# Optimization experiments

Hardware: AMD Instinct MI355X
Metric: run time of the kernel (lower is better)

The kernel has to match this reference:

```python
import jax, jax.numpy as jnp
import numpy as np

N_NODES = 10000
N_RAND_EDGES = 320000
IN_DIM = 256
HIDDEN = 64
HEADS = 8
OUT_DIM = 256
NEG_SLOPE = 0.2


def setup_inputs() -> dict:
    key = jax.random.key(0)
    ks = jax.random.split(key, 9)
    h = jax.random.normal(ks[0], (N_NODES, IN_DIM), dtype=jnp.float32)
    # random edges + self-loops so every dst has >=1 incoming edge
    src = jnp.concatenate([
        jax.random.randint(ks[1], (N_RAND_EDGES,), 0, N_NODES, dtype=jnp.int32),
        jnp.arange(N_NODES, dtype=jnp.int32)])
    dst = jnp.concatenate([
        jax.random.randint(ks[2], (N_RAND_EDGES,), 0, N_NODES, dtype=jnp.int32),
        jnp.arange(N_NODES, dtype=jnp.int32)])
    def glorot(k, shape):
        fan = shape[0] + shape[-1]
        s = jnp.sqrt(2.0 / fan).astype(jnp.float32)
        return jax.random.normal(k, shape, dtype=jnp.float32) * s
    W1 = glorot(ks[3], (IN_DIM, HEADS * HIDDEN))
    attn_l1 = glorot(ks[4], (HEADS, HIDDEN))
    attn_r1 = glorot(ks[5], (HEADS, HIDDEN))
    W2 = glorot(ks[6], (HEADS * HIDDEN, OUT_DIM))
    attn_l2 = glorot(ks[7], (1, OUT_DIM))
    attn_r2 = glorot(ks[8], (1, OUT_DIM))
    return {"h": h, "W1": W1, "attn_l1": attn_l1, "attn_r1": attn_r1,
            "W2": W2, "attn_l2": attn_l2, "attn_r2": attn_r2,
            "src": src, "dst": dst}


def gat_conv(x, W, attn_l, attn_r, src, dst, n_nodes):
    # x: [N, F_in]; W: [F_in, H*D]; attn_l/attn_r: [H, D]
    H, D = attn_l.shape
    feat = (x @ W).reshape(n_nodes, H, D)          # [N, H, D]
    el = jnp.einsum('nhd,hd->nh', feat, attn_l)    # [N, H]
    er = jnp.einsum('nhd,hd->nh', feat, attn_r)
    e = jax.nn.leaky_relu(el[src] + er[dst], NEG_SLOPE)  # [E, H]
    # edge softmax over incoming edges of each destination node
    m = jax.ops.segment_max(e, dst, num_segments=n_nodes)      # [N, H]
    ex = jnp.exp(e - m[dst])                                   # [E, H]
    denom = jax.ops.segment_sum(ex, dst, num_segments=n_nodes) # [N, H]
    alpha = ex / denom[dst]                                    # [E, H]
    out = jax.ops.segment_sum(alpha[:, :, None] * feat[src], dst,
                              num_segments=n_nodes)            # [N, H, D]
    return out.reshape(n_nodes, H * D)


def reference(h, W1, attn_l1, attn_r1, W2, attn_l2, attn_r2, src, dst):
    n = h.shape[0]
    x = gat_conv(h, W1, attn_l1, attn_r1, src, dst, n)   # [N, H*hidden]
    x = jax.nn.elu(x)
    out = gat_conv(x, W2, attn_l2, attn_r2, src, dst, n) # [N, out_dim]
    return out
```

## Files before the change

### kernel.cpp

```cpp
#include <hip/hip_runtime.h>
#include <hip/hip_bf16.h>

#define N_NODES 10000
#define IN_DIM 256
#define HID 512
#define HEADS 8
#define OUT_DIM 256
#define NEG 0.2f
#define CAP 128
#define WPREP_BLOCKS (((IN_DIM*HID)+(HID*OUT_DIM))/256)

typedef __hip_bfloat16 bf16;
typedef __attribute__((ext_vector_type(8))) short short8;
typedef __attribute__((ext_vector_type(4))) float f32x4;

__device__ __forceinline__ float ldm(const void* p, long i, int mode){
  if(mode) return ((const float*)p)[i];
  return __bfloat162float(((const bf16*)p)[i]);
}
__device__ __forceinline__ unsigned short f2bf(float f){
  bf16 b = __float2bfloat16(f);
  return *(unsigned short*)&b;
}
__device__ __forceinline__ float bflo(unsigned int u){ return __uint_as_float(u<<16); }
__device__ __forceinline__ float bfhi(unsigned int u){ return __uint_as_float(u&0xffff0000u); }

__global__ void detect_zero_k(const unsigned short* w1raw, int* mode, int* cnt,
                              float* el2, float* er2){
  int t = threadIdx.x;
  if(blockIdx.x==0){
    __shared__ int sbad;
    if(t==0) sbad=0;
    __syncthreads();
    int bad=0;
    for(int i=t;i<512;i+=256){
      unsigned int u = ((unsigned int)w1raw[i])<<16;
      float f = __uint_as_float(u);
      if(!(f==f) || fabsf(f) > 100.0f) bad++;
    }
    #pragma unroll
    for(int o=32;o>0;o>>=1) bad += __shfl_down(bad,o);
    if((t&63)==0) atomicAdd(&sbad, bad);
    __syncthreads();
    if(t==0) *mode = (sbad>10) ? 1 : 0;
  } else {
    int i = (blockIdx.x-1)*256 + t;
    if(i<N_NODES){ cnt[i]=0; el2[i]=0.f; er2[i]=0.f; }
  }
}

__global__ void prep2_k(const void* W1, const void* W2, unsigned short* wt1,
                        unsigned short* wt2, const int* modep,
                        const int* src, const int* dst, int* cnt, int* bucket, int E){
  int b = blockIdx.x, t = threadIdx.x;
  if(b < WPREP_BLOCKS){
    int md = *modep;
    long i = (long)b*256 + t;
    const long n1 = (long)IN_DIM*HID;
    if(i < n1){
      int k = (int)(i/HID), n = (int)(i%HID);
      unsigned short v = md ? f2bf(((const float*)W1)[i]) : ((const unsigned short*)W1)[i];
      wt1[(long)n*IN_DIM + k] = v;
    } else {
      long j = i - n1;
      int k = (int)(j/OUT_DIM), n = (int)(j%OUT_DIM);
      unsigned short v = md ? f2bf(((const float*)W2)[j]) : ((const unsigned short*)W2)[j];
      wt2[(long)n*HID + k] = v;
    }
  } else {
    int e = (b-WPREP_BLOCKS)*256 + t;
    if(e<E){
      int d = dst[e];
      int pos = atomicAdd(&cnt[d], 1);
      if(pos < CAP) bucket[(long)d*CAP + pos] = src[e];
    }
  }
}

__global__ __launch_bounds__(256) void gemm_k(const void* A, const unsigned short* Bt,
                                              unsigned short* C, int M, int N, int K,
                                              int asel, const int* modep,
                                              const void* al, const void* ar,
                                              float* el, float* er, int dmode){
  int md = *modep;
  int am = asel ? md : 0;
  __shared__ short As[64*40];
  __shared__ short Bs[64*40];
  __shared__ float led[64], ler[64];
  int t = threadIdx.x;
  int lane = t & 63, wave = t >> 6;
  int l15 = lane & 15, quad = lane >> 4;
  int wm = (wave>>1)*32, wn = (wave&1)*32;
  int mbase = blockIdx.y*64, nbase = blockIdx.x*64;

  f32x4 acc[2][2];
  #pragma unroll
  for(int i=0;i<2;i++)
    #pragma unroll
    for(int j=0;j<2;j++) acc[i][j] = (f32x4){0.f,0.f,0.f,0.f};

  int row = t>>2, kk = (t&3)*8;
  long arow = (long)(mbase+row)*K, brow = (long)(nbase+row)*K;
  bool av = (mbase+row) < M;
  const unsigned short* Ab = (const unsigned short*)A;
  const float* Af = (const float*)A;

  for(int k0=0;k0<K;k0+=32){
    short8 a = (short8){0,0,0,0,0,0,0,0};
    if(am){
      if(av){
        float4 x = *(const float4*)(Af + arow + k0 + kk);
        float4 y = *(const float4*)(Af + arow + k0 + kk + 4);
        a[0]=f2bf(x.x); a[1]=f2bf(x.y); a[2]=f2bf(x.z); a[3]=f2bf(x.w);
        a[4]=f2bf(y.x); a[5]=f2bf(y.y); a[6]=f2bf(y.z); a[7]=f2bf(y.w);
      }
    } else {
      if(av) a = *(const short8*)(Ab + arow + k0 + kk);
    }
    short8 b = *(const short8*)(Bt + brow + k0 + kk);
    __syncthreads();
    *(short8*)(As + row*40 + kk) = a;
    *(short8*)(Bs + row*40 + kk) = b;
    __syncthreads();
    short8 af[2], bfr[2];
    #pragma unroll
    for(int mi=0;mi<2;mi++) af[mi]  = *(short8*)(As + (wm + mi*16 + l15)*40 + quad*8);
    #pragma unroll
    for(int ni=0;ni<2;ni++) bfr[ni] = *(short8*)(Bs + (wn + ni*16 + l15)*40 + quad*8);
    #pragma unroll
    for(int mi=0;mi<2;mi++)
      #pragma unroll
      for(int ni=0;ni<2;ni++)
        acc[mi][ni] = __builtin_amdgcn_mfma_f32_16x16x32_bf16(af[mi], bfr[ni], acc[mi][ni], 0,0,0);
  }

  #pragma unroll
  for(int mi=0;mi<2;mi++){
    #pragma unroll
    for(int ni=0;ni<2;ni++){
      int grow0 = mbase + wm + mi*16 + quad*4;
      int gcol  = nbase + wn + ni*16 + l15;
      #pragma unroll
      for(int r=0;r<4;r++){
        int grow = grow0 + r;
        if(grow < M) C[(long)grow*N + gcol] = f2bf(acc[mi][ni][r]);
      }
    }
  }

  float avv[2], rvv[2];
  #pragma unroll
  for(int ni=0;ni<2;ni++){
    int gc = nbase + wn + ni*16 + l15;
    avv[ni] = ldm(al, gc, md);
    rvv[ni] = ldm(ar, gc, md);
  }
  __syncthreads();
  if(t<64){ led[t]=0.f; ler[t]=0.f; }
  __syncthreads();
  #pragma unroll
  for(int mi=0;mi<2;mi++){
    #pragma unroll
    for(int r=0;r<4;r++){
      float pl = acc[mi][0][r]*avv[0] + acc[mi][1][r]*avv[1];
      float pr = acc[mi][0][r]*rvv[0] + acc[mi][1][r]*rvv[1];
      #pragma unroll
      for(int o=1;o<16;o<<=1){ pl += __shfl_xor(pl,o); pr += __shfl_xor(pr,o); }
      if(l15==0){
        int lr = wm + mi*16 + quad*4 + r;
        atomicAdd(&led[lr], pl);
        atomicAdd(&ler[lr], pr);
      }
    }
  }
  __syncthreads();
  if(t<64){
    int grow = mbase + t;
    if(grow < M){
      if(dmode==1){
        el[(long)grow*HEADS + blockIdx.x] = led[t];
        er[(long)grow*HEADS + blockIdx.x] = ler[t];
      } else {
        atomicAdd(&el[grow], led[t]);
        atomicAdd(&er[grow], ler[t]);
      }
    }
  }
}

__global__ __launch_bounds__(64) void agg1_k(const unsigned short* fb, const float* el,
                       const float* er, const int* cnt, const int* bucket, unsigned short* x){
  int b = blockIdx.x;
  int ch = b / N_NODES;
  int n  = b - ch*N_NODES;
  int t = threadIdx.x;
  long off = (long)n*CAP;
  int deg = cnt[n]; if(deg>CAP) deg=CAP;
  __shared__ int sidx[CAP];
  __shared__ float wl[4][CAP];
  for(int i=t;i<deg;i+=64) sidx[i]=bucket[off+i];
  __syncthreads();
  int h0 = ch*4;
  float4 erv = *(const float4*)(er + (long)n*HEADS + h0);
  float pw0=0.f, pw1=0.f, pw2=0.f, pw3=0.f;
  for(int i=t;i<deg;i+=64){
    int s = sidx[i];
    float4 ev = *(const float4*)(el + (long)s*HEADS + h0);
    float e0 = ev.x + erv.x; e0 = e0>0.f?e0:NEG*e0;
    float e1 = ev.y + erv.y; e1 = e1>0.f?e1:NEG*e1;
    float e2 = ev.z + erv.z; e2 = e2>0.f?e2:NEG*e2;
    float e3 = ev.w + erv.w; e3 = e3>0.f?e3:NEG*e3;
    float wa = __expf(e0), wb = __expf(e1), wc = __expf(e2), wd = __expf(e3);
    wl[0][i]=wa; wl[1][i]=wb; wl[2][i]=wc; wl[3][i]=wd;
    pw0+=wa; pw1+=wb; pw2+=wc; pw3+=wd;
  }
  #pragma unroll
  for(int o=32;o>0;o>>=1){
    pw0 += __shfl_xor(pw0,o); pw1 += __shfl_xor(pw1,o);
    pw2 += __shfl_xor(pw2,o); pw3 += __shfl_xor(pw3,o);
  }
  float invs[4];
  invs[0] = pw0>0.f?1.f/pw0:0.f; invs[1] = pw1>0.f?1.f/pw1:0.f;
  invs[2] = pw2>0.f?1.f/pw2:0.f; invs[3] = pw3>0.f?1.f/pw3:0.f;
  __syncthreads();
  int hl = t>>4;
  int c0 = ch*256 + 4*t;
  const float* wsel = wl[hl];
  float inv = invs[hl];
  float a0=0.f,a1=0.f,a2=0.f,a3=0.f;
  #pragma unroll 4
  for(int i=0;i<deg;i++){
    int s = sidx[i];
    float w = wsel[i];
    uint2 u = *(const uint2*)(fb + (long)s*HID + c0);
    a0 += w*bflo(u.x); a1 += w*bfhi(u.x);
    a2 += w*bflo(u.y); a3 += w*bfhi(u.y);
  }
  a0*=inv; a1*=inv; a2*=inv; a3*=inv;
  a0 = a0>0.f ? a0 : __expf(a0)-1.f;
  a1 = a1>0.f ? a1 : __expf(a1)-1.f;
  a2 = a2>0.f ? a2 : __expf(a2)-1.f;
  a3 = a3>0.f ? a3 : __expf(a3)-1.f;
  uint2 o2;
  o2.x = (unsigned int)f2bf(a0) | ((unsigned int)f2bf(a1)<<16);
  o2.y = (unsigned int)f2bf(a2) | ((unsigned int)f2bf(a3)<<16);
  *(uint2*)(x + (long)n*HID + c0) = o2;
}

__global__ __launch_bounds__(64) void agg2_k(const unsigned short* fb, const float* el,
                       const float* er, const int* cnt, const int* bucket, void* out,
                       const int* modep){
  int md = *modep;
  int n = blockIdx.x, t = threadIdx.x;
  long off = (long)n*CAP;
  int deg = cnt[n]; if(deg>CAP) deg=CAP;
  __shared__ int sidx[CAP];
  __shared__ float wl[CAP];
  for(int i=t;i<deg;i+=64) sidx[i]=bucket[off+i];
  __syncthreads();
  float ern = er[n];
  float pw = 0.f;
  for(int i=t;i<deg;i+=64){
    int s = sidx[i];
    float e = el[s]+ern; e = e>0.f ? e : NEG*e;
    float w = __expf(e);
    wl[i]=w;
    pw += w;
  }
  #pragma unroll
  for(int o=32;o>0;o>>=1) pw += __shfl_xor(pw,o);
  float inv = pw>0.f ? 1.f/pw : 0.f;
  __syncthreads();
  int c0 = 4*t;
  float a0=0.f,a1=0.f,a2=0.f,a3=0.f;
  #pragma unroll 4
  for(int i=0;i<deg;i++){
    int s = sidx[i];
    float w = wl[i];
    uint2 u = *(const uint2*)(fb + (long)s*OUT_DIM + c0);
    a0 += w*bflo(u.x); a1 += w*bfhi(u.x);
    a2 += w*bflo(u.y); a3 += w*bfhi(u.y);
  }
  a0*=inv; a1*=inv; a2*=inv; a3*=inv;
  long oi = (long)n*OUT_DIM + c0;
  if(md){
    float4 fo; fo.x=a0; fo.y=a1; fo.z=a2; fo.w=a3;
    *(float4*)((float*)out + oi) = fo;
  } else {
    uint2 o2;
    o2.x = (unsigned int)f2bf(a0) | ((unsigned int)f2bf(a1)<<16);
    o2.y = (unsigned int)f2bf(a2) | ((unsigned int)f2bf(a3)<<16);
    *(uint2*)((unsigned short*)out + oi) = o2;
  }
}

extern "C" void kernel_launch(void* const* d_in, const int* in_sizes, int n_in,
                              void* d_out, int out_size, void* d_ws, size_t ws_size,
                              hipStream_t stream){
  (void)n_in; (void)out_size; (void)ws_size;
  const void* h_in = d_in[0];
  const void* W1   = d_in[1];
  const void* al1  = d_in[2];
  const void* ar1  = d_in[3];
  const void* W2   = d_in[4];
  const void* al2  = d_in[5];
  const void* ar2  = d_in[6];
  const int* src = (const int*)d_in[7];
  const int* dst = (const int*)d_in[8];
  int E = in_sizes[7];

  char* ws = (char*)d_ws;
  size_t o = 0;
  auto alloc = [&](size_t b){ size_t c=o; o += (b+255)&~(size_t)255; return c; };
  unsigned short* f1b  = (unsigned short*)(ws + alloc((size_t)N_NODES*HID*2));
  unsigned short* f2b  = (unsigned short*)(ws + alloc((size_t)N_NODES*OUT_DIM*2));
  unsigned short* xbuf = (unsigned short*)(ws + alloc((size_t)N_NODES*HID*2));
  unsigned short* wt1  = (unsigned short*)(ws + alloc((size_t)IN_DIM*HID*2));
  unsigned short* wt2  = (unsigned short*)(ws + alloc((size_t)HID*OUT_DIM*2));
  float* el1   = (float*)(ws + alloc((size_t)N_NODES*HEADS*4));
  float* er1   = (float*)(ws + alloc((size_t)N_NODES*HEADS*4));
  float* el2   = (float*)(ws + alloc((size_t)N_NODES*4));
  float* er2   = (float*)(ws + alloc((size_t)N_NODES*4));
  int* cnt     = (int*)(ws + alloc((size_t)N_NODES*4));
  int* bucket  = (int*)(ws + alloc((size_t)N_NODES*CAP*4));
  int* modep   = (int*)(ws + alloc(256));

  detect_zero_k<<<1+(N_NODES+255)/256,256,0,stream>>>(
      (const unsigned short*)W1, modep, cnt, el2, er2);
  prep2_k<<<WPREP_BLOCKS+(E+255)/256,256,0,stream>>>(
      W1, W2, wt1, wt2, modep, src, dst, cnt, bucket, E);

  gemm_k<<<dim3(HID/64,(N_NODES+63)/64),256,0,stream>>>(
      h_in, wt1, f1b, N_NODES, HID, IN_DIM, 1, modep, al1, ar1, el1, er1, 1);
  agg1_k<<<2*N_NODES,64,0,stream>>>(f1b, el1, er1, cnt, bucket, xbuf);

  gemm_k<<<dim3(OUT_DIM/64,(N_NODES+63)/64),256,0,stream>>>(
      xbuf, wt2, f2b, N_NODES, OUT_DIM, HID, 0, modep, al2, ar2, el2, er2, 2);
  agg2_k<<<N_NODES,64,0,stream>>>(f2b, el2, er2, cnt, bucket, d_out, modep);
}
```

Measured before the change: 184.5 us.

## Merge agg1 head chunks into one block per node; store layer-2 logit partials

The first-layer aggregation now runs one 64-thread block per node covering all 8 heads, not two blocks of 4 heads each. Each thread gathers 8 bf16 values with 16-byte loads, and the edge weights and softmax computation are shared across both halves. The second-layer attention logits are no longer accumulated with global atomics. Each GEMM column-block writes its own partial, agg2 sums the four partials when it reads them, and the zero-init of el2/er2 is removed. Fewer blocks per node means less parallelism across the grid, while the wider loads improve memory efficiency.

```diff
diff --git a/kernel.cpp b/kernel.cpp
--- a/kernel.cpp
+++ b/kernel.cpp
@@ -25,8 +25,7 @@
 __device__ __forceinline__ float bflo(unsigned int u){ return __uint_as_float(u<<16); }
 __device__ __forceinline__ float bfhi(unsigned int u){ return __uint_as_float(u&0xffff0000u); }
 
-__global__ void detect_zero_k(const unsigned short* w1raw, int* mode, int* cnt,
-                              float* el2, float* er2){
+__global__ void detect_zero_k(const unsigned short* w1raw, int* mode, int* cnt){
   int t = threadIdx.x;
   if(blockIdx.x==0){
     __shared__ int sbad;
@@ -45,7 +44,7 @@
     if(t==0) *mode = (sbad>10) ? 1 : 0;
   } else {
     int i = (blockIdx.x-1)*256 + t;
-    if(i<N_NODES){ cnt[i]=0; el2[i]=0.f; er2[i]=0.f; }
+    if(i<N_NODES) cnt[i]=0;
   }
 }
 
@@ -181,8 +180,8 @@
         el[(long)grow*HEADS + blockIdx.x] = led[t];
         er[(long)grow*HEADS + blockIdx.x] = ler[t];
       } else {
-        atomicAdd(&el[grow], led[t]);
-        atomicAdd(&er[grow], ler[t]);
+        el[(long)blockIdx.x*N_NODES + grow] = led[t];
+        er[(long)blockIdx.x*N_NODES + grow] = ler[t];
       }
     }
   }
@@ -190,65 +189,77 @@
 
 __global__ __launch_bounds__(64) void agg1_k(const unsigned short* fb, const float* el,
                        const float* er, const int* cnt, const int* bucket, unsigned short* x){
-  int b = blockIdx.x;
-  int ch = b / N_NODES;
-  int n  = b - ch*N_NODES;
+  int n = blockIdx.x;
   int t = threadIdx.x;
   long off = (long)n*CAP;
   int deg = cnt[n]; if(deg>CAP) deg=CAP;
   __shared__ int sidx[CAP];
-  __shared__ float wl[4][CAP];
+  __shared__ float wl[CAP][8];
+  __shared__ float sinv[8];
   for(int i=t;i<deg;i+=64) sidx[i]=bucket[off+i];
   __syncthreads();
-  int h0 = ch*4;
-  float4 erv = *(const float4*)(er + (long)n*HEADS + h0);
-  float pw0=0.f, pw1=0.f, pw2=0.f, pw3=0.f;
+  float4 erA = *(const float4*)(er + (long)n*HEADS);
+  float4 erB = *(const float4*)(er + (long)n*HEADS + 4);
+  float pw[8];
+  #pragma unroll
+  for(int h=0;h<8;h++) pw[h]=0.f;
   for(int i=t;i<deg;i+=64){
     int s = sidx[i];
-    float4 ev = *(const float4*)(el + (long)s*HEADS + h0);
-    float e0 = ev.x + erv.x; e0 = e0>0.f?e0:NEG*e0;
-    float e1 = ev.y + erv.y; e1 = e1>0.f?e1:NEG*e1;
-    float e2 = ev.z + erv.z; e2 = e2>0.f?e2:NEG*e2;
-    float e3 = ev.w + erv.w; e3 = e3>0.f?e3:NEG*e3;
-    float wa = __expf(e0), wb = __expf(e1), wc = __expf(e2), wd = __expf(e3);
-    wl[0][i]=wa; wl[1][i]=wb; wl[2][i]=wc; wl[3][i]=wd;
-    pw0+=wa; pw1+=wb; pw2+=wc; pw3+=wd;
-  }
-  #pragma unroll
-  for(int o=32;o>0;o>>=1){
-    pw0 += __shfl_xor(pw0,o); pw1 += __shfl_xor(pw1,o);
-    pw2 += __shfl_xor(pw2,o); pw3 += __shfl_xor(pw3,o);
-  }
-  float invs[4];
-  invs[0] = pw0>0.f?1.f/pw0:0.f; invs[1] = pw1>0.f?1.f/pw1:0.f;
-  invs[2] = pw2>0.f?1.f/pw2:0.f; invs[3] = pw3>0.f?1.f/pw3:0.f;
-  __syncthreads();
-  int hl = t>>4;
-  int c0 = ch*256 + 4*t;
-  const float* wsel = wl[hl];
-  float inv = invs[hl];
-  float a0=0.f,a1=0.f,a2=0.f,a3=0.f;
+    float4 eA = *(const float4*)(el + (long)s*HEADS);
+    float4 eB = *(const float4*)(el + (long)s*HEADS + 4);
+    float ee[8] = {eA.x+erA.x, eA.y+erA.y, eA.z+erA.z, eA.w+erA.w,
+                   eB.x+erB.x, eB.y+erB.y, eB.z+erB.z, eB.w+erB.w};
+    #pragma unroll
+    for(int h=0;h<8;h++){
+      float e = ee[h]; e = e>0.f ? e : NEG*e;
+      float w = __expf(e);
+      wl[i][h]=w;
+      pw[h]+=w;
+    }
+  }
+  #pragma unroll
+  for(int h=0;h<8;h++){
+    #pragma unroll
+    for(int o=32;o>0;o>>=1) pw[h] += __shfl_xor(pw[h],o);
+  }
+  if(t==0){
+    #pragma unroll
+    for(int h=0;h<8;h++) sinv[h] = pw[h]>0.f ? 1.f/pw[h] : 0.f;
+  }
+  __syncthreads();
+  int hl = t>>3;
+  float inv = sinv[hl];
+  int c0 = 8*t;
+  float a0=0.f,a1=0.f,a2=0.f,a3=0.f,a4=0.f,a5=0.f,a6=0.f,a7=0.f;
   #pragma unroll 4
   for(int i=0;i<deg;i++){
     int s = sidx[i];
-    float w = wsel[i];
-    uint2 u = *(const uint2*)(fb + (long)s*HID + c0);
+    float w = wl[i][hl];
+    uint4 u = *(const uint4*)(fb + (long)s*HID + c0);
     a0 += w*bflo(u.x); a1 += w*bfhi(u.x);
     a2 += w*bflo(u.y); a3 += w*bfhi(u.y);
-  }
-  a0*=inv; a1*=inv; a2*=inv; a3*=inv;
+    a4 += w*bflo(u.z); a5 += w*bfhi(u.z);
+    a6 += w*bflo(u.w); a7 += w*bfhi(u.w);
+  }
+  a0*=inv; a1*=inv; a2*=inv; a3*=inv; a4*=inv; a5*=inv; a6*=inv; a7*=inv;
   a0 = a0>0.f ? a0 : __expf(a0)-1.f;
   a1 = a1>0.f ? a1 : __expf(a1)-1.f;
   a2 = a2>0.f ? a2 : __expf(a2)-1.f;
   a3 = a3>0.f ? a3 : __expf(a3)-1.f;
-  uint2 o2;
-  o2.x = (unsigned int)f2bf(a0) | ((unsigned int)f2bf(a1)<<16);
-  o2.y = (unsigned int)f2bf(a2) | ((unsigned int)f2bf(a3)<<16);
-  *(uint2*)(x + (long)n*HID + c0) = o2;
-}
-
-__global__ __launch_bounds__(64) void agg2_k(const unsigned short* fb, const float* el,
-                       const float* er, const int* cnt, const int* bucket, void* out,
+  a4 = a4>0.f ? a4 : __expf(a4)-1.f;
+  a5 = a5>0.f ? a5 : __expf(a5)-1.f;
+  a6 = a6>0.f ? a6 : __expf(a6)-1.f;
+  a7 = a7>0.f ? a7 : __expf(a7)-1.f;
+  uint4 o4;
+  o4.x = (unsigned int)f2bf(a0) | ((unsigned int)f2bf(a1)<<16);
+  o4.y = (unsigned int)f2bf(a2) | ((unsigned int)f2bf(a3)<<16);
+  o4.z = (unsigned int)f2bf(a4) | ((unsigned int)f2bf(a5)<<16);
+  o4.w = (unsigned int)f2bf(a6) | ((unsigned int)f2bf(a7)<<16);
+  *(uint4*)(x + (long)n*HID + c0) = o4;
+}
+
+__global__ __launch_bounds__(64) void agg2_k(const unsigned short* fb, const float* elp,
+                       const float* erp, const int* cnt, const int* bucket, void* out,
                        const int* modep){
   int md = *modep;
   int n = blockIdx.x, t = threadIdx.x;
@@ -258,11 +269,12 @@
   __shared__ float wl[CAP];
   for(int i=t;i<deg;i+=64) sidx[i]=bucket[off+i];
   __syncthreads();
-  float ern = er[n];
+  float ern = erp[n] + erp[N_NODES+n] + erp[2*N_NODES+n] + erp[3*N_NODES+n];
   float pw = 0.f;
   for(int i=t;i<deg;i+=64){
     int s = sidx[i];
-    float e = el[s]+ern; e = e>0.f ? e : NEG*e;
+    float e = elp[s] + elp[N_NODES+s] + elp[2*N_NODES+s] + elp[3*N_NODES+s] + ern;
+    e = e>0.f ? e : NEG*e;
     float w = __expf(e);
     wl[i]=w;
     pw += w;
@@ -319,22 +331,22 @@
   unsigned short* wt2  = (unsigned short*)(ws + alloc((size_t)HID*OUT_DIM*2));
   float* el1   = (float*)(ws + alloc((size_t)N_NODES*HEADS*4));
   float* er1   = (float*)(ws + alloc((size_t)N_NODES*HEADS*4));
-  float* el2   = (float*)(ws + alloc((size_t)N_NODES*4));
-  float* er2   = (float*)(ws + alloc((size_t)N_NODES*4));
+  float* el2p  = (float*)(ws + alloc((size_t)4*N_NODES*4));
+  float* er2p  = (float*)(ws + alloc((size_t)4*N_NODES*4));
   int* cnt     = (int*)(ws + alloc((size_t)N_NODES*4));
   int* bucket  = (int*)(ws + alloc((size_t)N_NODES*CAP*4));
   int* modep   = (int*)(ws + alloc(256));
 
   detect_zero_k<<<1+(N_NODES+255)/256,256,0,stream>>>(
-      (const unsigned short*)W1, modep, cnt, el2, er2);
+      (const unsigned short*)W1, modep, cnt);
   prep2_k<<<WPREP_BLOCKS+(E+255)/256,256,0,stream>>>(
       W1, W2, wt1, wt2, modep, src, dst, cnt, bucket, E);
 
   gemm_k<<<dim3(HID/64,(N_NODES+63)/64),256,0,stream>>>(
       h_in, wt1, f1b, N_NODES, HID, IN_DIM, 1, modep, al1, ar1, el1, er1, 1);
-  agg1_k<<<2*N_NODES,64,0,stream>>>(f1b, el1, er1, cnt, bucket, xbuf);
+  agg1_k<<<N_NODES,64,0,stream>>>(f1b, el1, er1, cnt, bucket, xbuf);
 
   gemm_k<<<dim3(OUT_DIM/64,(N_NODES+63)/64),256,0,stream>>>(
-      xbuf, wt2, f2b, N_NODES, OUT_DIM, HID, 0, modep, al2, ar2, el2, er2, 2);
-  agg2_k<<<N_NODES,64,0,stream>>>(f2b, el2, er2, cnt, bucket, d_out, modep);
-}
+      xbuf, wt2, f2b, N_NODES, OUT_DIM, HID, 0, modep, al2, ar2, el2p, er2p, 2);
+  agg2_k<<<N_NODES,64,0,stream>>>(f2b, el2p, er2p, cnt, bucket, d_out, modep);
+}
```

After: 194.8 us. 5.6% more time.
